# Performance work log

Measured on AMD Instinct MI355X. Metric: run time of the kernel, lower is better.

Reference implementation:

```python
import jax, jax.numpy as jnp
import numpy as np

Z = Y = X = 128
H = W = 256
FEAT_CH = 128
PE_DIM = 9
EMB = 128
B, V, NPTS = 2, 4, 65536


def make_grid_zyx():
    zs = jnp.linspace(-1.0, 1.0, Z)
    ys = jnp.linspace(-1.0, 1.0, Y)
    xs = jnp.linspace(-1.0, 1.0, X)
    gz, gy, gx = jnp.meshgrid(zs, ys, xs, indexing='ij')
    return jnp.stack([gz, gy, gx], axis=-1).reshape(-1, 3)  # (Z*Y*X, 3)


def fourier_pe(c):
    # coords + sin/cos at base frequency -> 3+3+3 = 9 dims
    return jnp.concatenate([c, jnp.sin(jnp.pi * c), jnp.cos(jnp.pi * c)], axis=-1)


def bilinear_sample(fm, py, px):
    # fm: (C,H,W); py,px: (n,) pixel coords (align_corners, border clamp) -> (n,C)
    px = jnp.clip(px, 0.0, W - 1.0)
    py = jnp.clip(py, 0.0, H - 1.0)
    x0 = jnp.clip(jnp.floor(px).astype(jnp.int32), 0, W - 2)
    y0 = jnp.clip(jnp.floor(py).astype(jnp.int32), 0, H - 2)
    x1, y1 = x0 + 1, y0 + 1
    wx = px - x0
    wy = py - y0
    f00 = fm[:, y0, x0]; f01 = fm[:, y0, x1]
    f10 = fm[:, y1, x0]; f11 = fm[:, y1, x1]
    top = f00 * (1.0 - wx) + f01 * wx
    bot = f10 * (1.0 - wx) + f11 * wx
    return (top * (1.0 - wy) + bot * wy).T


def inr_mlp(x, w_in, b_in, w1, b1, w2, b2, w_out, b_out):
    # pre-act residual MLP: num_blocks is small & static, loop is fine
    h = jax.nn.relu(x @ w_in + b_in)
    for i in range(w1.shape[0]):
        h = jax.nn.relu(h + jax.nn.relu(h @ w1[i] + b1[i]) @ w2[i] + b2[i])
    return h @ w_out + b_out


def setup_inputs() -> dict:
    key = jax.random.key(0)
    ks = jax.random.split(key, 24)
    s = 0.05
    n = lambda k, shp: jax.random.normal(k, shp, jnp.float32) * s
    return {
        'views': jax.random.normal(ks[0], (B, V, 1, H, W), jnp.float32),
        'angles': jax.random.uniform(ks[1], (B, V), jnp.float32, 0.0, 2.0 * np.pi),
        'idx': jax.random.randint(ks[2], (NPTS,), 0, Z * Y * X, jnp.int32),
        'conv_w': n(ks[3], (FEAT_CH, 1, 3, 3)),
        'conv_b': n(ks[4], (FEAT_CH,)),
        'vw_in': n(ks[5], (FEAT_CH + PE_DIM, 128)), 'vb_in': n(ks[6], (128,)),
        'vw1': n(ks[7], (3, 128, 128)), 'vb1': n(ks[8], (3, 128)),
        'vw2': n(ks[9], (3, 128, 128)), 'vb2': n(ks[10], (3, 128)),
        'vw_out': n(ks[11], (128, EMB)), 'vb_out': n(ks[12], (EMB,)),
        'gw_in': n(ks[13], (EMB, 128)), 'gb_in': n(ks[14], (128,)),
        'gw1': n(ks[15], (2, 128, 128)), 'gb1': n(ks[16], (2, 128)),
        'gw2': n(ks[17], (2, 128, 128)), 'gb2': n(ks[18], (2, 128)),
        'gw_out': n(ks[19], (128, 1)), 'gb_out': n(ks[20], (1,)),
    }


def reference(views, angles, idx, conv_w, conv_b, vw_in, vb_in, vw1, vb1, vw2, vb2,
              vw_out, vb_out, gw_in, gb_in, gw1, gb1, gw2, gb2, gw_out, gb_out):
    Bn, Vn = views.shape[0], views.shape[1]
    npts = idx.shape[0]
    # backbone (U-Net stand-in): 3x3 conv 1->feat_ch + ReLU
    x2d = views.reshape(Bn * Vn, 1, H, W)
    feats = jax.lax.conv_general_dilated(x2d, conv_w, (1, 1), 'SAME',
                                         dimension_numbers=('NCHW', 'OIHW', 'NCHW'))
    feats = jax.nn.relu(feats + conv_b[None, :, None, None]).reshape(Bn, Vn, FEAT_CH, H, W)
    # gather coords for requested voxels, positional encoding
    coords = make_grid_zyx()[idx]                      # (n,3) zyx in [-1,1]
    pe = fourier_pe(coords)                            # (n,9)
    z, y, x = coords[:, 0], coords[:, 1], coords[:, 2]
    ct = jnp.cos(angles)[..., None]                    # (B,V,1)
    st = jnp.sin(angles)[..., None]
    u = x[None, None, :] * ct - y[None, None, :] * st  # rotated in-plane coord (B,V,n)
    v = jnp.broadcast_to(z[None, None, :], u.shape)    # detector vertical = z
    px = (u + 1.0) * 0.5 * (W - 1)
    py = (v + 1.0) * 0.5 * (H - 1)
    f = jax.vmap(jax.vmap(bilinear_sample))(feats, py, px)        # (B,V,n,C)
    pe_b = jnp.broadcast_to(pe[None, None], (Bn, Vn, npts, PE_DIM))
    xin = jnp.concatenate([f, pe_b], axis=-1).reshape(Bn * Vn * npts, FEAT_CH + PE_DIM)
    r = inr_mlp(xin, vw_in, vb_in, vw1, vb1, vw2, vb2, vw_out, vb_out)
    r_mean = r.reshape(Bn, Vn, npts, EMB).mean(axis=1)            # sum over views / V
    yout = inr_mlp(r_mean.reshape(Bn * npts, EMB), gw_in, gb_in, gw1, gb1, gw2, gb2, gw_out, gb_out)
    return yout.reshape(Bn, npts)
```

## Files before the change

kernel.cpp:

```cpp
#include <hip/hip_runtime.h>
#include <math.h>

#define BB 2
#define VV 4
#define NPTSC 65536
#define HH 256
#define WW 256
#define CCH 128
#define PTS 32
#define ROWS (VV * PTS)

typedef __attribute__((ext_vector_type(8))) unsigned short ushort8;
typedef __attribute__((ext_vector_type(4))) unsigned short u16x4;
typedef __attribute__((ext_vector_type(8))) __bf16 bf16x8;
typedef __attribute__((ext_vector_type(4))) float floatx4;

__device__ unsigned short g_feats[(size_t)BB * VV * HH * WW * CCH];

__device__ __forceinline__ float b2f(unsigned short u) {
  unsigned int x = ((unsigned int)u) << 16;
  return __builtin_bit_cast(float, x);
}
__device__ __forceinline__ unsigned short f2b(float f) {
  return __builtin_bit_cast(unsigned short, (__bf16)f);
}

__global__ __launch_bounds__(256) void mvct_pc(
    const float* __restrict__ views, const float* __restrict__ conv_w,
    const float* __restrict__ conv_b,
    const float* __restrict__ vw_in, const float* __restrict__ vw1,
    const float* __restrict__ vw2, const float* __restrict__ vw_out,
    const float* __restrict__ gw_in, const float* __restrict__ gw1,
    const float* __restrict__ gw2, unsigned short* __restrict__ wbuf)
{
  if (blockIdx.x < 1024) {
    __shared__ float rows[2][3][258];
    const int half = threadIdx.x >> 7;
    const int c = threadIdx.x & 127;
    const int bv = blockIdx.x >> 7;
    const int y = ((blockIdx.x & 127) << 1) | half;

    float w[9];
#pragma unroll
    for (int j = 0; j < 9; ++j) w[j] = conv_w[c * 9 + j];
    float bias = conv_b[c];

    const float* img = views + (size_t)bv * HH * WW;
#pragma unroll
    for (int r = 0; r < 3; ++r) {
      int yy = y - 1 + r;
      for (int x = c; x < 258; x += 128) {
        int xx = x - 1;
        float v = 0.f;
        if (yy >= 0 && yy < HH && xx >= 0 && xx < WW) v = img[yy * WW + xx];
        rows[half][r][x] = v;
      }
    }
    __syncthreads();

    unsigned short* orow = g_feats + ((size_t)(bv * HH + y) * WW) * CCH + c;
    for (int x = 0; x < WW; ++x) {
      float acc = bias;
#pragma unroll
      for (int r = 0; r < 3; ++r)
#pragma unroll
        for (int d = 0; d < 3; ++d)
          acc += rows[half][r][x + d] * w[r * 3 + d];
      acc = fmaxf(acc, 0.f);
      orow[(size_t)x * CCH] = f2b(acc);
    }
  } else {
    int tid = (blockIdx.x - 1024) * 256 + threadIdx.x;
    if (tid >= 217088) return;
    float val;
    if (tid < 20480) {
      int n = tid / 160, k = tid - n * 160;
      val = (k < 137) ? vw_in[k * 128 + n] : 0.f;
    } else {
      int t = tid - 20480;
      const float* src;
      if (t < 49152) { src = vw1; }
      else if (t < 98304) { t -= 49152; src = vw2; }
      else if (t < 114688) { t -= 98304; src = vw_out; }
      else if (t < 131072) { t -= 114688; src = gw_in; }
      else if (t < 163840) { t -= 131072; src = gw1; }
      else { t -= 163840; src = gw2; }
      int i = t >> 14; int r = t & 16383; int n = r >> 7; int k = r & 127;
      val = src[i * 16384 + k * 128 + n];
    }
    wbuf[tid] = f2b(val);
  }
}

struct WReg {
  ushort8 a[2][4];
  floatx4 bs[2];
};

__device__ __forceinline__ WReg wload(const unsigned short* __restrict__ Wt,
                                      const float* __restrict__ bias,
                                      int lane, int ftBase) {
  WReg w;
  const int col = lane & 15, quad = lane >> 4;
#pragma unroll
  for (int ftl = 0; ftl < 2; ++ftl) {
    const int ft = ftBase + ftl;
#pragma unroll
    for (int kk = 0; kk < 4; ++kk)
      w.a[ftl][kk] = *(const ushort8*)(Wt + (ft * 16 + col) * 128 + kk * 32 + quad * 8);
    w.bs[ftl] = *(const floatx4*)(bias + ft * 16 + quad * 4);
  }
  return w;
}

template<int MODE, int NPT>
__device__ __forceinline__ void mlp_c(
    const unsigned short* Act, int lda, const WReg& w,
    const unsigned short* Res, int ldr,
    unsigned short* Dst, int ldd,
    float* racc, int lane, int ftBase)
{
  const int col = lane & 15, quad = lane >> 4;
  auto body = [&](int ptt) {
    ushort8 bfr[4];
#pragma unroll
    for (int kk = 0; kk < 4; ++kk)
      bfr[kk] = *(const ushort8*)(Act + (ptt * 16 + col) * lda + kk * 32 + quad * 8);
#pragma unroll
    for (int ftl = 0; ftl < 2; ++ftl) {
      const int ft = ftBase + ftl;
      floatx4 acc = {0.f, 0.f, 0.f, 0.f};
#pragma unroll
      for (int kk = 0; kk < 4; ++kk)
        acc = __builtin_amdgcn_mfma_f32_16x16x32_bf16(
            __builtin_bit_cast(bf16x8, w.a[ftl][kk]),
            __builtin_bit_cast(bf16x8, bfr[kk]), acc, 0, 0, 0);
      const int row = ptt * 16 + col;
      if constexpr (MODE == 2) {
#pragma unroll
        for (int r = 0; r < 4; ++r)
          racc[(ptt & 1) * 8 + ftl * 4 + r] += acc[r] + w.bs[ftl][r];
      } else {
        u16x4 rv;
        if constexpr (MODE == 1)
          rv = *(const u16x4*)(Res + row * ldr + ft * 16 + quad * 4);
        u16x4 o;
#pragma unroll
        for (int r = 0; r < 4; ++r) {
          float v = acc[r] + w.bs[ftl][r];
          if constexpr (MODE == 1) v += b2f(rv[r]);
          v = fmaxf(v, 0.f);
          o[r] = f2b(v);
        }
        *(u16x4*)(Dst + row * ldd + ft * 16 + quad * 4) = o;
      }
    }
  };
  if constexpr (MODE == 2) {
#pragma unroll
    for (int ptt = 0; ptt < NPT; ++ptt) body(ptt);
  } else {
#pragma unroll 2
    for (int ptt = 0; ptt < NPT; ++ptt) body(ptt);
  }
  __syncthreads();
}

__device__ __forceinline__ void mlp_first(
    const unsigned short* Act, int lda,
    const unsigned short* __restrict__ Wt, const float* __restrict__ bias,
    unsigned short* Dst, int ldd, int lane, int ftBase)
{
  const int col = lane & 15, quad = lane >> 4;
  ushort8 afr[2][5];
  floatx4 bs4[2];
#pragma unroll
  for (int ftl = 0; ftl < 2; ++ftl) {
    const int ft = ftBase + ftl;
#pragma unroll
    for (int kk = 0; kk < 5; ++kk)
      afr[ftl][kk] = *(const ushort8*)(Wt + (ft * 16 + col) * 160 + kk * 32 + quad * 8);
    bs4[ftl] = *(const floatx4*)(bias + ft * 16 + quad * 4);
  }
#pragma unroll 2
  for (int ptt = 0; ptt < (ROWS / 16); ++ptt) {
    ushort8 bfr[5];
#pragma unroll
    for (int kk = 0; kk < 5; ++kk)
      bfr[kk] = *(const ushort8*)(Act + (ptt * 16 + col) * lda + kk * 32 + quad * 8);
#pragma unroll
    for (int ftl = 0; ftl < 2; ++ftl) {
      const int ft = ftBase + ftl;
      floatx4 acc = {0.f, 0.f, 0.f, 0.f};
#pragma unroll
      for (int kk = 0; kk < 5; ++kk)
        acc = __builtin_amdgcn_mfma_f32_16x16x32_bf16(
            __builtin_bit_cast(bf16x8, afr[ftl][kk]),
            __builtin_bit_cast(bf16x8, bfr[kk]), acc, 0, 0, 0);
      const int row = ptt * 16 + col;
      u16x4 o;
#pragma unroll
      for (int r = 0; r < 4; ++r)
        o[r] = f2b(fmaxf(acc[r] + bs4[ftl][r], 0.f));
      *(u16x4*)(Dst + row * ldd + ft * 16 + quad * 4) = o;
    }
  }
  __syncthreads();
}

__global__ __launch_bounds__(256, 2) void mvct_main(
    const float* __restrict__ angles, const int* __restrict__ idx,
    const unsigned short* __restrict__ wbuf,
    const float* __restrict__ vb_in, const float* __restrict__ vb1,
    const float* __restrict__ vb2, const float* __restrict__ vb_out,
    const float* __restrict__ gb_in, const float* __restrict__ gb1,
    const float* __restrict__ gb2, const float* __restrict__ gw_out,
    const float* __restrict__ gb_out,
    float* __restrict__ out)
{
  __shared__ __align__(16) unsigned short X[ROWS][168];
  __shared__ __align__(16) unsigned short Hb[ROWS][136];
  const int tid = threadIdx.x;
  const int lane = tid & 63;
  const int ftBase = (tid >> 6) * 2;
  const int b = blockIdx.x >> 11;
  const int pts0 = (blockIdx.x & 2047) * PTS;

  const unsigned short* w_in_t   = wbuf;
  const unsigned short* vw1_t    = wbuf + 20480;
  const unsigned short* vw2_t    = wbuf + 69632;
  const unsigned short* vw_out_t = wbuf + 118784;
  const unsigned short* gw_in_t  = wbuf + 135168;
  const unsigned short* gw1_t    = wbuf + 151552;
  const unsigned short* gw2_t    = wbuf + 184320;

  const float inv = 2.0f / 127.0f;
  const int col = lane & 15, quad = lane >> 4;

  if (tid < ROWS) {
    int p = tid & (PTS - 1);
    int id = idx[pts0 + p];
    int iz = (id >> 14) & 127, iy = (id >> 7) & 127, ix = id & 127;
    float x = ix * inv - 1.f, y = iy * inv - 1.f, z = iz * inv - 1.f;
    const float PI = 3.14159265358979323846f;
    float pe[9] = {z, y, x, sinf(PI * z), sinf(PI * y), sinf(PI * x),
                   cosf(PI * z), cosf(PI * y), cosf(PI * x)};
#pragma unroll
    for (int j = 0; j < 9; ++j) X[tid][128 + j] = f2b(pe[j]);
    for (int j = 137; j < 160; ++j) X[tid][j] = 0;
  }

#pragma unroll
  for (int v = 0; v < VV; ++v) {
    const int bv = b * VV + v;
    const float ang = angles[bv];
    const float ct = cosf(ang), st = sinf(ang);
    const int cg = tid & 15;
#pragma unroll
    for (int ph = 0; ph < 2; ++ph) {
      const int p = ((tid >> 4) & 15) + ph * 16;
      int id = idx[pts0 + p];
      int iz = (id >> 14) & 127, iy = (id >> 7) & 127, ix = id & 127;
      float x = ix * inv - 1.f, y = iy * inv - 1.f, z = iz * inv - 1.f;
      float u = x * ct - y * st;
      float px = (u + 1.f) * 127.5f, py = (z + 1.f) * 127.5f;
      px = fminf(fmaxf(px, 0.f), 255.f);
      py = fminf(fmaxf(py, 0.f), 255.f);
      int x0 = min((int)px, 254), y0 = min((int)py, 254);
      float wx = px - (float)x0, wy = py - (float)y0;
      const unsigned short* bp =
          g_feats + ((size_t)((bv * HH + y0) * WW + x0)) * CCH + cg * 8;
      ushort8 q00 = *(const ushort8*)bp;
      ushort8 q01 = *(const ushort8*)(bp + CCH);
      ushort8 q10 = *(const ushort8*)(bp + WW * CCH);
      ushort8 q11 = *(const ushort8*)(bp + WW * CCH + CCH);
      float w00 = (1.f - wx) * (1.f - wy), w01 = wx * (1.f - wy);
      float w10 = (1.f - wx) * wy, w11 = wx * wy;
      ushort8 o;
#pragma unroll
      for (int j = 0; j < 8; ++j) {
        float f = w00 * b2f(q00[j]) + w01 * b2f(q01[j]) +
                  w10 * b2f(q10[j]) + w11 * b2f(q11[j]);
        o[j] = f2b(f);
      }
      *(ushort8*)&X[v * PTS + p][cg * 8] = o;
    }
  }
  __syncthreads();

  float racc[16];
#pragma unroll
  for (int i = 0; i < 16; ++i) racc[i] = 0.f;

  WReg wA = wload(vw1_t, vb1, lane, ftBase);
  mlp_first(&X[0][0], 168, w_in_t, vb_in, &Hb[0][0], 136, lane, ftBase);
  WReg wB = wload(vw2_t, vb2, lane, ftBase);
  mlp_c<0, 8>(&Hb[0][0], 136, wA, nullptr, 0, &X[0][0], 168, nullptr,
              lane, ftBase);
  wA = wload(vw1_t + 16384, vb1 + 128, lane, ftBase);
  mlp_c<1, 8>(&X[0][0], 168, wB, &Hb[0][0], 136, &Hb[0][0], 136, nullptr,
              lane, ftBase);
  wB = wload(vw2_t + 16384, vb2 + 128, lane, ftBase);
  mlp_c<0, 8>(&Hb[0][0], 136, wA, nullptr, 0, &X[0][0], 168, nullptr,
              lane, ftBase);
  wA = wload(vw1_t + 32768, vb1 + 256, lane, ftBase);
  mlp_c<1, 8>(&X[0][0], 168, wB, &Hb[0][0], 136, &Hb[0][0], 136, nullptr,
              lane, ftBase);
  wB = wload(vw2_t + 32768, vb2 + 256, lane, ftBase);
  mlp_c<0, 8>(&Hb[0][0], 136, wA, nullptr, 0, &X[0][0], 168, nullptr,
              lane, ftBase);
  wA = wload(vw_out_t, vb_out, lane, ftBase);
  mlp_c<1, 8>(&X[0][0], 168, wB, &Hb[0][0], 136, &Hb[0][0], 136, nullptr,
              lane, ftBase);
  wB = wload(gw_in_t, gb_in, lane, ftBase);
  mlp_c<2, 8>(&Hb[0][0], 136, wA, nullptr, 0, nullptr, 0, racc,
              lane, ftBase);

#pragma unroll
  for (int ph = 0; ph < 2; ++ph)
#pragma unroll
    for (int ftl = 0; ftl < 2; ++ftl) {
      u16x4 o;
#pragma unroll
      for (int r = 0; r < 4; ++r)
        o[r] = f2b(racc[ph * 8 + ftl * 4 + r] * 0.25f);
      *(u16x4*)(&X[ph * 16 + col][(ftBase + ftl) * 16 + quad * 4]) = o;
    }
  __syncthreads();

  wA = wload(gw1_t, gb1, lane, ftBase);
  mlp_c<0, 2>(&X[0][0], 168, wB, nullptr, 0, &Hb[0][0], 136, nullptr,
              lane, ftBase);
  wB = wload(gw2_t, gb2, lane, ftBase);
  mlp_c<0, 2>(&Hb[0][0], 136, wA, nullptr, 0, &X[0][0], 168, nullptr,
              lane, ftBase);
  wA = wload(gw1_t + 16384, gb1 + 128, lane, ftBase);
  mlp_c<1, 2>(&X[0][0], 168, wB, &Hb[0][0], 136, &Hb[0][0], 136, nullptr,
              lane, ftBase);
  wB = wload(gw2_t + 16384, gb2 + 128, lane, ftBase);
  mlp_c<0, 2>(&Hb[0][0], 136, wA, nullptr, 0, &X[0][0], 168, nullptr,
              lane, ftBase);
  mlp_c<1, 2>(&X[0][0], 168, wB, &Hb[0][0], 136, &Hb[0][0], 136, nullptr,
              lane, ftBase);

  if (tid < 128) {
    const int p = (tid & 15) + ((tid >> 6) << 4);
    const int q4 = (tid >> 4) & 3;
    float s = 0.f;
    const unsigned short* hr = &Hb[p][q4 * 32];
    const float* wo = gw_out + q4 * 32;
#pragma unroll
    for (int c = 0; c < 32; ++c)
      s += b2f(hr[c]) * wo[c];
    s += __shfl_xor(s, 16, 64);
    s += __shfl_xor(s, 32, 64);
    if (q4 == 0)
      out[(size_t)b * NPTSC + pts0 + p] = s + gb_out[0];
  }
}

extern "C" void kernel_launch(void* const* d_in, const int* in_sizes, int n_in,
                              void* d_out, int out_size, void* d_ws, size_t ws_size,
                              hipStream_t stream) {
  const float* views  = (const float*)d_in[0];
  const float* angles = (const float*)d_in[1];
  const int*   idx    = (const int*)d_in[2];
  const float* conv_w = (const float*)d_in[3];
  const float* conv_b = (const float*)d_in[4];
  const float* vw_in  = (const float*)d_in[5];
  const float* vb_in  = (const float*)d_in[6];
  const float* vw1    = (const float*)d_in[7];
  const float* vb1    = (const float*)d_in[8];
  const float* vw2    = (const float*)d_in[9];
  const float* vb2    = (const float*)d_in[10];
  const float* vw_out = (const float*)d_in[11];
  const float* vb_out = (const float*)d_in[12];
  const float* gw_in  = (const float*)d_in[13];
  const float* gb_in  = (const float*)d_in[14];
  const float* gw1    = (const float*)d_in[15];
  const float* gb1    = (const float*)d_in[16];
  const float* gw2    = (const float*)d_in[17];
  const float* gb2    = (const float*)d_in[18];
  const float* gw_out = (const float*)d_in[19];
  const float* gb_out = (const float*)d_in[20];

  unsigned short* wbuf = (unsigned short*)d_ws;

  hipLaunchKernelGGL(mvct_pc, dim3(1872), dim3(256), 0, stream,
                     views, conv_w, conv_b,
                     vw_in, vw1, vw2, vw_out, gw_in, gw1, gw2, wbuf);
  hipLaunchKernelGGL(mvct_main, dim3(BB * (NPTSC / PTS)), dim3(256), 0, stream,
                     angles, idx, wbuf, vb_in, vb1, vb2, vb_out,
                     gb_in, gb1, gb2, gw_out, gb_out,
                     (float*)d_out);
}
```

Measured before the change: 406.0 us.

## Split MLP rows across two wave groups with 512-thread blocks

Doubles the block to 512 threads. Each wave now handles half of the point-rows for its two feature tiles, so per-wave MFMA work per layer halves and more waves are resident. The per-view reduction of the first MLP's output is now combined across the two row halves through fp32 scratch in shared memory. The bilinear gather is reorganised so each thread decodes one point and loops over views. LDS row strides change to 170/138 to shift bank mapping. Risks: these strides break 16-byte alignment of the vector LDS accesses, the 512×4 launch bound squeezes registers and may cause spills, and the extra barriers add cost.

```diff
diff --git a/kernel.cpp b/kernel.cpp
--- a/kernel.cpp
+++ b/kernel.cpp
@@ -9,6 +9,8 @@
 #define CCH 128
 #define PTS 32
 #define ROWS (VV * PTS)
+#define LDA 170
+#define LDH 138
 
 typedef __attribute__((ext_vector_type(8))) unsigned short ushort8;
 typedef __attribute__((ext_vector_type(4))) unsigned short u16x4;
@@ -118,14 +120,15 @@
     const unsigned short* Act, int lda, const WReg& w,
     const unsigned short* Res, int ldr,
     unsigned short* Dst, int ldd,
-    float* racc, int lane, int ftBase)
+    float* racc, int lane, int ftBase, int rowBase)
 {
   const int col = lane & 15, quad = lane >> 4;
   auto body = [&](int ptt) {
+    const int row = rowBase + ptt * 16 + col;
     ushort8 bfr[4];
 #pragma unroll
     for (int kk = 0; kk < 4; ++kk)
-      bfr[kk] = *(const ushort8*)(Act + (ptt * 16 + col) * lda + kk * 32 + quad * 8);
+      bfr[kk] = *(const ushort8*)(Act + row * lda + kk * 32 + quad * 8);
 #pragma unroll
     for (int ftl = 0; ftl < 2; ++ftl) {
       const int ft = ftBase + ftl;
@@ -135,7 +138,6 @@
         acc = __builtin_amdgcn_mfma_f32_16x16x32_bf16(
             __builtin_bit_cast(bf16x8, w.a[ftl][kk]),
             __builtin_bit_cast(bf16x8, bfr[kk]), acc, 0, 0, 0);
-      const int row = ptt * 16 + col;
       if constexpr (MODE == 2) {
 #pragma unroll
         for (int r = 0; r < 4; ++r)
@@ -169,7 +171,7 @@
 __device__ __forceinline__ void mlp_first(
     const unsigned short* Act, int lda,
     const unsigned short* __restrict__ Wt, const float* __restrict__ bias,
-    unsigned short* Dst, int ldd, int lane, int ftBase)
+    unsigned short* Dst, int ldd, int lane, int ftBase, int rowBase)
 {
   const int col = lane & 15, quad = lane >> 4;
   ushort8 afr[2][5];
@@ -183,11 +185,12 @@
     bs4[ftl] = *(const floatx4*)(bias + ft * 16 + quad * 4);
   }
 #pragma unroll 2
-  for (int ptt = 0; ptt < (ROWS / 16); ++ptt) {
+  for (int ptt = 0; ptt < 4; ++ptt) {
+    const int row = rowBase + ptt * 16 + col;
     ushort8 bfr[5];
 #pragma unroll
     for (int kk = 0; kk < 5; ++kk)
-      bfr[kk] = *(const ushort8*)(Act + (ptt * 16 + col) * lda + kk * 32 + quad * 8);
+      bfr[kk] = *(const ushort8*)(Act + row * lda + kk * 32 + quad * 8);
 #pragma unroll
     for (int ftl = 0; ftl < 2; ++ftl) {
       const int ft = ftBase + ftl;
@@ -197,7 +200,6 @@
         acc = __builtin_amdgcn_mfma_f32_16x16x32_bf16(
             __builtin_bit_cast(bf16x8, afr[ftl][kk]),
             __builtin_bit_cast(bf16x8, bfr[kk]), acc, 0, 0, 0);
-      const int row = ptt * 16 + col;
       u16x4 o;
 #pragma unroll
       for (int r = 0; r < 4; ++r)
@@ -208,7 +210,7 @@
   __syncthreads();
 }
 
-__global__ __launch_bounds__(256, 2) void mvct_main(
+__global__ __launch_bounds__(512, 4) void mvct_main(
     const float* __restrict__ angles, const int* __restrict__ idx,
     const unsigned short* __restrict__ wbuf,
     const float* __restrict__ vb_in, const float* __restrict__ vb1,
@@ -218,11 +220,14 @@
     const float* __restrict__ gb_out,
     float* __restrict__ out)
 {
-  __shared__ __align__(16) unsigned short X[ROWS][168];
-  __shared__ __align__(16) unsigned short Hb[ROWS][136];
+  __shared__ __align__(16) unsigned short X[ROWS][LDA];
+  __shared__ __align__(16) unsigned short Hb[ROWS][LDH];
   const int tid = threadIdx.x;
   const int lane = tid & 63;
-  const int ftBase = (tid >> 6) * 2;
+  const int wav = tid >> 6;
+  const int rh = wav >> 2;
+  const int ftBase = (wav & 3) * 2;
+  const int rowBase = rh * 64;
   const int b = blockIdx.x >> 11;
   const int pts0 = (blockIdx.x & 2047) * PTS;
 
@@ -250,18 +255,17 @@
     for (int j = 137; j < 160; ++j) X[tid][j] = 0;
   }
 
-#pragma unroll
-  for (int v = 0; v < VV; ++v) {
-    const int bv = b * VV + v;
-    const float ang = angles[bv];
-    const float ct = cosf(ang), st = sinf(ang);
+  {
     const int cg = tid & 15;
-#pragma unroll
-    for (int ph = 0; ph < 2; ++ph) {
-      const int p = ((tid >> 4) & 15) + ph * 16;
-      int id = idx[pts0 + p];
-      int iz = (id >> 14) & 127, iy = (id >> 7) & 127, ix = id & 127;
-      float x = ix * inv - 1.f, y = iy * inv - 1.f, z = iz * inv - 1.f;
+    const int p = (tid >> 4) & 31;
+    const int id = idx[pts0 + p];
+    const int iz = (id >> 14) & 127, iy = (id >> 7) & 127, ix = id & 127;
+    const float x = ix * inv - 1.f, y = iy * inv - 1.f, z = iz * inv - 1.f;
+#pragma unroll
+    for (int v = 0; v < VV; ++v) {
+      const int bv = b * VV + v;
+      const float ang = angles[bv];
+      const float ct = cosf(ang), st = sinf(ang);
       float u = x * ct - y * st;
       float px = (u + 1.f) * 127.5f, py = (z + 1.f) * 127.5f;
       px = fminf(fmaxf(px, 0.f), 255.f);
@@ -293,55 +297,73 @@
   for (int i = 0; i < 16; ++i) racc[i] = 0.f;
 
   WReg wA = wload(vw1_t, vb1, lane, ftBase);
-  mlp_first(&X[0][0], 168, w_in_t, vb_in, &Hb[0][0], 136, lane, ftBase);
+  mlp_first(&X[0][0], LDA, w_in_t, vb_in, &Hb[0][0], LDH, lane, ftBase, rowBase);
   WReg wB = wload(vw2_t, vb2, lane, ftBase);
-  mlp_c<0, 8>(&Hb[0][0], 136, wA, nullptr, 0, &X[0][0], 168, nullptr,
-              lane, ftBase);
+  mlp_c<0, 4>(&Hb[0][0], LDH, wA, nullptr, 0, &X[0][0], LDA, nullptr,
+              lane, ftBase, rowBase);
   wA = wload(vw1_t + 16384, vb1 + 128, lane, ftBase);
-  mlp_c<1, 8>(&X[0][0], 168, wB, &Hb[0][0], 136, &Hb[0][0], 136, nullptr,
-              lane, ftBase);
+  mlp_c<1, 4>(&X[0][0], LDA, wB, &Hb[0][0], LDH, &Hb[0][0], LDH, nullptr,
+              lane, ftBase, rowBase);
   wB = wload(vw2_t + 16384, vb2 + 128, lane, ftBase);
-  mlp_c<0, 8>(&Hb[0][0], 136, wA, nullptr, 0, &X[0][0], 168, nullptr,
-              lane, ftBase);
+  mlp_c<0, 4>(&Hb[0][0], LDH, wA, nullptr, 0, &X[0][0], LDA, nullptr,
+              lane, ftBase, rowBase);
   wA = wload(vw1_t + 32768, vb1 + 256, lane, ftBase);
-  mlp_c<1, 8>(&X[0][0], 168, wB, &Hb[0][0], 136, &Hb[0][0], 136, nullptr,
-              lane, ftBase);
+  mlp_c<1, 4>(&X[0][0], LDA, wB, &Hb[0][0], LDH, &Hb[0][0], LDH, nullptr,
+              lane, ftBase, rowBase);
   wB = wload(vw2_t + 32768, vb2 + 256, lane, ftBase);
-  mlp_c<0, 8>(&Hb[0][0], 136, wA, nullptr, 0, &X[0][0], 168, nullptr,
-              lane, ftBase);
+  mlp_c<0, 4>(&Hb[0][0], LDH, wA, nullptr, 0, &X[0][0], LDA, nullptr,
+              lane, ftBase, rowBase);
   wA = wload(vw_out_t, vb_out, lane, ftBase);
-  mlp_c<1, 8>(&X[0][0], 168, wB, &Hb[0][0], 136, &Hb[0][0], 136, nullptr,
-              lane, ftBase);
+  mlp_c<1, 4>(&X[0][0], LDA, wB, &Hb[0][0], LDH, &Hb[0][0], LDH, nullptr,
+              lane, ftBase, rowBase);
   wB = wload(gw_in_t, gb_in, lane, ftBase);
-  mlp_c<2, 8>(&Hb[0][0], 136, wA, nullptr, 0, nullptr, 0, racc,
-              lane, ftBase);
-
-#pragma unroll
-  for (int ph = 0; ph < 2; ++ph)
-#pragma unroll
-    for (int ftl = 0; ftl < 2; ++ftl) {
-      u16x4 o;
-#pragma unroll
-      for (int r = 0; r < 4; ++r)
-        o[r] = f2b(racc[ph * 8 + ftl * 4 + r] * 0.25f);
-      *(u16x4*)(&X[ph * 16 + col][(ftBase + ftl) * 16 + quad * 4]) = o;
-    }
+  mlp_c<2, 4>(&Hb[0][0], LDH, wA, nullptr, 0, nullptr, 0, racc,
+              lane, ftBase, rowBase);
+
+  wA = wload(gw1_t, gb1, lane, ftBase);
+  float* scr = (float*)((char*)&X[0][0] + 32 * LDA * 2);
+  if (rh == 1) {
+#pragma unroll
+    for (int ph = 0; ph < 2; ++ph)
+#pragma unroll
+      for (int ftl = 0; ftl < 2; ++ftl) {
+        floatx4 v4;
+#pragma unroll
+        for (int r = 0; r < 4; ++r) v4[r] = racc[ph * 8 + ftl * 4 + r];
+        *(floatx4*)&scr[(ph * 16 + col) * 132 + (ftBase + ftl) * 16 + quad * 4] = v4;
+      }
+  }
   __syncthreads();
-
-  wA = wload(gw1_t, gb1, lane, ftBase);
-  mlp_c<0, 2>(&X[0][0], 168, wB, nullptr, 0, &Hb[0][0], 136, nullptr,
-              lane, ftBase);
+  if (rh == 0) {
+#pragma unroll
+    for (int ph = 0; ph < 2; ++ph)
+#pragma unroll
+      for (int ftl = 0; ftl < 2; ++ftl) {
+        floatx4 pv = *(const floatx4*)&scr[(ph * 16 + col) * 132 +
+                                           (ftBase + ftl) * 16 + quad * 4];
+        u16x4 o;
+#pragma unroll
+        for (int r = 0; r < 4; ++r)
+          o[r] = f2b((racc[ph * 8 + ftl * 4 + r] + pv[r]) * 0.25f);
+        *(u16x4*)(&X[ph * 16 + col][(ftBase + ftl) * 16 + quad * 4]) = o;
+      }
+  }
+  __syncthreads();
+
+  const int gBase = rh * 16;
+  mlp_c<0, 1>(&X[0][0], LDA, wB, nullptr, 0, &Hb[0][0], LDH, nullptr,
+              lane, ftBase, gBase);
   wB = wload(gw2_t, gb2, lane, ftBase);
-  mlp_c<0, 2>(&Hb[0][0], 136, wA, nullptr, 0, &X[0][0], 168, nullptr,
-              lane, ftBase);
+  mlp_c<0, 1>(&Hb[0][0], LDH, wA, nullptr, 0, &X[0][0], LDA, nullptr,
+              lane, ftBase, gBase);
   wA = wload(gw1_t + 16384, gb1 + 128, lane, ftBase);
-  mlp_c<1, 2>(&X[0][0], 168, wB, &Hb[0][0], 136, &Hb[0][0], 136, nullptr,
-              lane, ftBase);
+  mlp_c<1, 1>(&X[0][0], LDA, wB, &Hb[0][0], LDH, &Hb[0][0], LDH, nullptr,
+              lane, ftBase, gBase);
   wB = wload(gw2_t + 16384, gb2 + 128, lane, ftBase);
-  mlp_c<0, 2>(&Hb[0][0], 136, wA, nullptr, 0, &X[0][0], 168, nullptr,
-              lane, ftBase);
-  mlp_c<1, 2>(&X[0][0], 168, wB, &Hb[0][0], 136, &Hb[0][0], 136, nullptr,
-              lane, ftBase);
+  mlp_c<0, 1>(&Hb[0][0], LDH, wA, nullptr, 0, &X[0][0], LDA, nullptr,
+              lane, ftBase, gBase);
+  mlp_c<1, 1>(&X[0][0], LDA, wB, &Hb[0][0], LDH, &Hb[0][0], LDH, nullptr,
+              lane, ftBase, gBase);
 
   if (tid < 128) {
     const int p = (tid & 15) + ((tid >> 6) << 4);
@@ -389,7 +411,7 @@
   hipLaunchKernelGGL(mvct_pc, dim3(1872), dim3(256), 0, stream,
                      views, conv_w, conv_b,
                      vw_in, vw1, vw2, vw_out, gw_in, gw1, gw2, wbuf);
-  hipLaunchKernelGGL(mvct_main, dim3(BB * (NPTSC / PTS)), dim3(256), 0, stream,
+  hipLaunchKernelGGL(mvct_main, dim3(BB * (NPTSC / PTS)), dim3(512), 0, stream,
                      angles, idx, wbuf, vb_in, vb1, vb2, vb_out,
                      gb_in, gb1, gb2, gw_out, gb_out,
                      (float*)d_out);
```

Result: slower. 1.139 ms (+180.5%).
